# Optimization experiments

Hardware: AMD Instinct MI355X
Metric: run time of the kernel (lower is better)

Reference implementation:

```python
import jax, jax.numpy as jnp
from jax import lax
import numpy as np

H = 180; W = 180            # BEV map: grid_size 1440 / out_size_factor 8
CIN = 384; C = 128; K = 10  # in_channels, hidden_channel, num_classes
P = 200; NH = 8; B = 2      # num_proposals, num_heads, batch
OUT_DIMS = (2, 1, 3, 2, 2, 10)  # center, height, dim, rot, vel, heatmap


def pos2embed(pos, nf=C):
    # faithful to MFFusionHead.pos2embed (note: temperature is unused in source)
    pos = pos * (2.0 * np.pi)
    dim_t = jnp.arange(nf, dtype=pos.dtype)
    dim_t = 2.0 * jnp.floor(dim_t / 2.0) / nf + 1.0
    px = pos[..., 0, None] / dim_t
    py = pos[..., 1, None] / dim_t
    def interleave(p):
        return jnp.stack((jnp.sin(p[..., 0::2]), jnp.cos(p[..., 1::2])), axis=-1).reshape(p.shape[:-1] + (nf,))
    return jnp.concatenate((interleave(py), interleave(px)), axis=-1)  # [..., 2*nf]


def conv2d(t, w, b):
    return lax.conv_general_dilated(t, w, (1, 1), 'SAME', dimension_numbers=('NCHW', 'OIHW', 'NCHW')) + b[None, :, None, None]


def conv1d(t, w, b):
    return lax.conv_general_dilated(t, w, (1,), 'SAME', dimension_numbers=('NCH', 'OIH', 'NCH')) + b[None, :, None]


def layernorm(t, g, b):
    m = t.mean(-1, keepdims=True)
    v = ((t - m) ** 2).mean(-1, keepdims=True)
    return g * (t - m) / jnp.sqrt(v + 1e-5) + b


def mha(q, k, v, w_in, b_in, w_o, b_o):
    Bq, Lq, Cq = q.shape
    d = Cq // NH
    qh = (q @ w_in[0] + b_in[0]).reshape(Bq, Lq, NH, d)
    kh = (k @ w_in[1] + b_in[1]).reshape(Bq, -1, NH, d)
    vh = (v @ w_in[2] + b_in[2]).reshape(Bq, -1, NH, d)
    att = jax.nn.softmax(jnp.einsum('bqhd,bkhd->bhqk', qh, kh) / float(np.sqrt(d)), axis=-1)
    o = jnp.einsum('bhqk,bkhd->bqhd', att, vh).reshape(Bq, Lq, Cq)
    return o @ w_o + b_o


def _forward(x, w_shared, b_shared, w_hm1, b_hm1, g_hm1, beta_hm1, w_hm2, b_hm2,
             w_fp1, b_fp1, g_fp1, beta_fp1, w_fp2, b_fp2,
             w_be1, b_be1, w_be2, b_be2,
             w_attn_s, b_attn_s, w_out_s, b_out_s,
             w_attn_c, b_attn_c, w_out_c, b_out_c,
             ln1_g, ln1_b, ln2_g, ln2_b, ln3_g, ln3_b,
             w_ff1, b_ff1, w_ff2, b_ff2,
             w_head1, b_head1, g_head1, beta_head1, w_head2, b_head2):
    Bx = x.shape[0]
    # shared 3x3 conv over fused BEV features
    feat = conv2d(x, w_shared, b_shared)                      # [B, C, H, W]

    def head2d(w1, b1, g, be, w2, b2):
        h = conv2d(feat, w1, b1)
        h = jax.nn.relu(g[None, :, None, None] * h + be[None, :, None, None])  # BN (eval, affine) + ReLU
        return conv2d(h, w2, b2)

    dense_hm = head2d(w_hm1, b_hm1, g_hm1, beta_hm1, w_hm2, b_hm2)  # [B, K, H, W]
    frontmap = head2d(w_fp1, b_fp1, g_fp1, beta_fp1, w_fp2, b_fp2)  # [B, 1, H, W] (aux output)
    del frontmap

    # local-max NMS on detached sigmoid heatmap
    hm = jax.nn.sigmoid(lax.stop_gradient(dense_hm))
    lm = lax.reduce_window(hm, -jnp.inf, lax.max, (1, 1, 3, 3), (1, 1, 1, 1), 'SAME')
    hm = hm * (hm == lm).astype(hm.dtype)

    # top-k proposal selection across (class, position)
    _, idx = lax.top_k(hm.reshape(Bx, -1), P)                 # [B, P]
    top_idx = idx % (H * W)

    feat_flat = feat.reshape(Bx, C, H * W)

    def gather(a, i):
        return jnp.take_along_axis(a, jnp.broadcast_to(i[:, None, :], (Bx, a.shape[1], P)), axis=2)

    query_feat = gather(feat_flat, top_idx)                   # [B, C, P]
    q_hm_score = gather(hm.reshape(Bx, K, H * W), top_idx)    # [B, K, P]

    # coords_bev grid (+0.5 centers), normalized for sinusoidal embedding
    bev = jnp.stack(jnp.meshgrid(jnp.arange(H, dtype=jnp.float32) + 0.5,
                                 jnp.arange(W, dtype=jnp.float32) + 0.5,
                                 indexing='ij'), axis=-1).reshape(-1, 2)
    bev_n = bev / jnp.asarray([H, W], jnp.float32)

    def emb(p):  # bev_embedding MLP on pos2embed
        return jax.nn.relu(pos2embed(p) @ w_be1 + b_be1) @ w_be2 + b_be2

    qpe = emb(bev_n[top_idx])                                 # [B, P, C]
    kpe = emb(bev_n)[None]                                    # [1, HW, C]

    q = query_feat.transpose(0, 2, 1)                         # [B, P, C]
    mem = feat_flat.transpose(0, 2, 1)                        # [B, HW, C]

    # decoder layer: self-attn -> cross-attn to BEV -> FFN (post-norm)
    q = layernorm(q + mha(q + qpe, q + qpe, q, w_attn_s, b_attn_s, w_out_s, b_out_s), ln1_g, ln1_b)
    q = layernorm(q + mha(q + qpe, mem + kpe, mem, w_attn_c, b_attn_c, w_out_c, b_out_c), ln2_g, ln2_b)
    q = layernorm(q + jax.nn.relu(q @ w_ff1 + b_ff1) @ w_ff2 + b_ff2, ln3_g, ln3_b)

    # SeparateHead prediction (Conv1d k=3 + BN + ReLU + Conv1d)
    qc = q.transpose(0, 2, 1)                                 # [B, C, P]
    outs = []
    for i, od in enumerate(OUT_DIMS):
        h = jax.nn.relu(g_head1[i][None, :, None] * conv1d(qc, w_head1[i], b_head1[i]) + beta_head1[i][None, :, None])
        outs.append(conv1d(h, w_head2[i, :od], b_head2[i, :od]))
    outs[5] = outs[5] + q_hm_score                            # fuse gathered heatmap score into class logits
    return jnp.concatenate(outs, axis=1)                      # [B, 20, P]


def setup_inputs() -> dict:
    key = jax.random.key(0)
    ks = iter(jax.random.split(key, 60))
    def rn(shape, s=0.02):
        return jax.random.normal(next(ks), shape, jnp.float32) * s
    return dict(
        x=jax.random.normal(next(ks), (B, CIN, H, W), jnp.float32),
        w_shared=rn((C, CIN, 3, 3)), b_shared=rn((C,)),
        w_hm1=rn((C, C, 3, 3)), b_hm1=rn((C,)), g_hm1=1.0 + rn((C,)), beta_hm1=rn((C,)),
        w_hm2=rn((K, C, 3, 3)), b_hm2=rn((K,)),
        w_fp1=rn((C, C, 3, 3)), b_fp1=rn((C,)), g_fp1=1.0 + rn((C,)), beta_fp1=rn((C,)),
        w_fp2=rn((1, C, 3, 3)), b_fp2=rn((1,)),
        w_be1=rn((2 * C, C)), b_be1=rn((C,)), w_be2=rn((C, C)), b_be2=rn((C,)),
        w_attn_s=rn((3, C, C)), b_attn_s=rn((3, C)), w_out_s=rn((C, C)), b_out_s=rn((C,)),
        w_attn_c=rn((3, C, C)), b_attn_c=rn((3, C)), w_out_c=rn((C, C)), b_out_c=rn((C,)),
        ln1_g=1.0 + rn((C,)), ln1_b=rn((C,)), ln2_g=1.0 + rn((C,)), ln2_b=rn((C,)),
        ln3_g=1.0 + rn((C,)), ln3_b=rn((C,)),
        w_ff1=rn((C, 2 * C)), b_ff1=rn((2 * C,)), w_ff2=rn((2 * C, C)), b_ff2=rn((C,)),
        w_head1=rn((6, C, C, 3)), b_head1=rn((6, C)), g_head1=1.0 + rn((6, C)), beta_head1=rn((6, C)),
        w_head2=rn((6, K, C, 3)), b_head2=rn((6, K)),
    )


def reference(x, w_shared, b_shared, w_hm1, b_hm1, g_hm1, beta_hm1, w_hm2, b_hm2,
              w_fp1, b_fp1, g_fp1, beta_fp1, w_fp2, b_fp2,
              w_be1, b_be1, w_be2, b_be2,
              w_attn_s, b_attn_s, w_out_s, b_out_s,
              w_attn_c, b_attn_c, w_out_c, b_out_c,
              ln1_g, ln1_b, ln2_g, ln2_b, ln3_g, ln3_b,
              w_ff1, b_ff1, w_ff2, b_ff2,
              w_head1, b_head1, g_head1, beta_head1, w_head2, b_head2):
    return _forward(x, w_shared, b_shared, w_hm1, b_hm1, g_hm1, beta_hm1, w_hm2, b_hm2,
                    w_fp1, b_fp1, g_fp1, beta_fp1, w_fp2, b_fp2,
                    w_be1, b_be1, w_be2, b_be2,
                    w_attn_s, b_attn_s, w_out_s, b_out_s,
                    w_attn_c, b_attn_c, w_out_c, b_out_c,
                    ln1_g, ln1_b, ln2_g, ln2_b, ln3_g, ln3_b,
                    w_ff1, b_ff1, w_ff2, b_ff2,
                    w_head1, b_head1, g_head1, beta_head1, w_head2, b_head2)
```

## Files before the change

kernel.cpp:

```cpp
#include <hip/hip_runtime.h>

#define HH 180
#define WW 180
#define HWN 32400
#define CC 128
#define CINN 384
#define KK 10
#define PP 200
#define NHH 8
#define BB 2
#define NTOT 324000
#define TKBINS (1 << 18)

typedef _Float16 half8 __attribute__((ext_vector_type(8)));
typedef float f32x16 __attribute__((ext_vector_type(16)));

static __device__ __forceinline__ f32x16 MFMA16(half8 a, half8 b, f32x16 c) {
    return __builtin_amdgcn_mfma_f32_32x32x16_f16(a, b, c, 0, 0, 0);
}

__global__ void k_wsplit(const float* __restrict__ w, _Float16* __restrict__ img, int cint) {
    const int e = blockIdx.x * 256 + threadIdx.x;
    const int total = (cint / 32) * 9 * 8192;
    if (e >= total) return;
    const int ii = e & 7, cout = (e >> 3) & 127, q = (e >> 10) & 3, t = (e >> 12) & 1;
    const int bidx = e >> 13, tap = bidx % 9, ch = bidx / 9;
    const int cin = ch * 32 + q * 8 + ii;
    const float v = w[((size_t)cout * cint + cin) * 9 + tap];
    const _Float16 h = (_Float16)v;
    img[e] = (t == 0) ? h : (_Float16)((v - (float)h) * 256.f);
}

__global__ void k_wsplit_hm(const float* __restrict__ w, _Float16* __restrict__ img) {
    const int e = blockIdx.x * 256 + threadIdx.x;
    const int total = 4 * 9 * 2048;
    if (e >= total) return;
    const int ii = e & 7, co = (e >> 3) & 31, q = (e >> 8) & 3, t = (e >> 10) & 1;
    const int bidx = e >> 11, tap = bidx % 9, ch = bidx / 9;
    const int cin = ch * 32 + q * 8 + ii;
    const float v = (co < 10) ? w[((size_t)co * 128 + cin) * 9 + tap] : 0.f;
    const _Float16 h = (_Float16)v;
    img[e] = (t == 0) ? h : (_Float16)((v - (float)h) * 256.f);
}

__global__ __launch_bounds__(256) void k_xsplit(const float* __restrict__ x,
    _Float16* __restrict__ out, int CIN, int NCH)
{
    __shared__ float tile[32][184];
    const int ch = blockIdx.x, y = blockIdx.y, b = blockIdx.z;
    const int tid = threadIdx.x;
    for (int s = tid; s < 32 * 180; s += 256) {
        const int c = s / 180, px = s % 180;
        tile[c][px] = x[(((size_t)b * CIN + ch * 32 + c) * HH + y) * WW + px];
    }
    __syncthreads();
    const size_t pbase = ((((size_t)b * 180 + y) * NCH + ch) * 2) * (180 * 32);
    for (int tt = tid; tt < 1440; tt += 256) {
        const int t = tt / 720, u = tt % 720, px = u >> 2, q = u & 3;
        half8 hv;
#pragma unroll
        for (int j = 0; j < 8; ++j) {
            const float v = tile[q * 8 + j][px];
            const _Float16 h = (_Float16)v;
            hv[j] = (t == 0) ? h : (_Float16)((v - (float)h) * 256.f);
        }
        *(half8*)(out + pbase + (size_t)t * (180 * 32) + px * 32 + q * 8) = hv;
    }
}

template<int NCH, int EPI, int WRITEF, int SPLIT>
__global__ __launch_bounds__(256, 3) void k_conv(
    const _Float16* __restrict__ xs, const _Float16* __restrict__ wimg,
    const float* __restrict__ bias, const float* __restrict__ g,
    const float* __restrict__ beta, float* __restrict__ outf,
    _Float16* __restrict__ outs)
{
    __shared__ __align__(16) char sh[36992];
    const int tid = threadIdx.x;
    const int b = blockIdx.z >> 1, ch2 = blockIdx.z & 1;
    const int oy0 = blockIdx.y * 2, ox0 = blockIdx.x * 64;
    const int wave = tid >> 6, l = tid & 63;
    const int wr = wave >> 1, nh = wave & 1;
    const int l31 = l & 31, kb = l >> 5;

    f32x16 acc1[2] = {};
    f32x16 acc2[2] = {};

    int wofs[2][2];
#pragma unroll
    for (int t = 0; t < 2; ++t)
#pragma unroll
        for (int s = 0; s < 2; ++s)
            wofs[t][s] = (((t * 4) + (s * 2 + kb)) * 128 + ch2 * 64 + nh * 32 + l31) * 16;

    half8 bwC[2][2], bwN[2][2];
#pragma unroll
    for (int t = 0; t < 2; ++t)
#pragma unroll
        for (int s = 0; s < 2; ++s)
            bwC[t][s] = *(const half8*)((const char*)wimg + wofs[t][s]);

#pragma unroll 1
    for (int ch = 0; ch < NCH; ++ch) {
        if (ch) __syncthreads();
#pragma unroll
        for (int k = 0; k < 9; ++k) {
            const int tt = tid + k * 256;
            if (tt < 2112) {
                const int seg = tt / 264, u = tt - seg * 264;
                const int t = seg >> 2, r = seg & 3;
                const int i = u >> 2, q = u & 3;
                const int gy = oy0 - 1 + r, gx = ox0 - 1 + i;
                uint4 v = {0u, 0u, 0u, 0u};
                if ((unsigned)gy < 180u && (unsigned)gx < 180u)
                    v = *(const uint4*)((const char*)xs +
                        (((((size_t)b * 180 + gy) * NCH + ch) * 2 + t) * 180 + gx) * 64 + q * 16);
                *(uint4*)(sh + ((t * 4 + r) * 4 + q) * 1056 + i * 16) = v;
            }
        }
        __syncthreads();
#pragma unroll
        for (int tap = 0; tap < 9; ++tap) {
            const int bidx = ch * 9 + tap;
            const bool pf = (bidx + 1 < NCH * 9);
            if (pf) {
                const char* wn = (const char*)wimg + (size_t)(bidx + 1) * 16384;
#pragma unroll
                for (int t = 0; t < 2; ++t)
#pragma unroll
                    for (int s = 0; s < 2; ++s)
                        bwN[t][s] = *(const half8*)(wn + wofs[t][s]);
            }
            const int ky = tap / 3, kx = tap % 3;
            const int rr = wr + ky;
#pragma unroll
            for (int s = 0; s < 2; ++s) {
                const int q = s * 2 + kb;
                half8 ah[2], al[2];
#pragma unroll
                for (int mf = 0; mf < 2; ++mf) {
                    const int io = (mf * 32 + l31 + kx) * 16;
                    ah[mf] = *(const half8*)(sh + ((rr) * 4 + q) * 1056 + io);
                    al[mf] = *(const half8*)(sh + ((4 + rr) * 4 + q) * 1056 + io);
                }
#pragma unroll
                for (int mf = 0; mf < 2; ++mf) {
                    acc1[mf] = MFMA16(ah[mf], bwC[0][s], acc1[mf]);
                    acc2[mf] = MFMA16(ah[mf], bwC[1][s], acc2[mf]);
                    acc2[mf] = MFMA16(al[mf], bwC[0][s], acc2[mf]);
                }
            }
            if (pf) {
#pragma unroll
                for (int t = 0; t < 2; ++t)
#pragma unroll
                    for (int s = 0; s < 2; ++s)
                        bwC[t][s] = bwN[t][s];
            }
        }
    }

    float* C = (float*)sh;
    const float inv256 = 1.f / 256.f;
    __syncthreads();
#pragma unroll
    for (int mf = 0; mf < 2; ++mf)
#pragma unroll
        for (int reg = 0; reg < 16; ++reg) {
            const int px = mf * 32 + (reg & 3) + 8 * (reg >> 2) + 4 * kb;
            const int co = nh * 32 + l31;
            C[(co * 2 + wr) * 72 + px] = acc1[mf][reg] + acc2[mf][reg] * inv256;
// ... 270 lines not shown
    __shared__ float pe[16][258];
    __shared__ float hid[16][130];
    const int tid = threadIdx.x;
    const int pos0 = blockIdx.x * 16;
    const int half = tid >> 6, m = tid & 63;
    const float dimt = 1.f + (float)m * 0.015625f;
#pragma unroll
    for (int p = 0; p < 16; ++p) {
        const int pos = pos0 + p;
        const int i = pos / WW, j = pos % WW;
        const float coord = (half == 0) ? ((float)j + 0.5f) * (1.f / 180.f)
                                        : ((float)i + 0.5f) * (1.f / 180.f);
        const float arg = (coord * 6.2831855f) / dimt;
        pe[p][half * 128 + 2 * m]     = sinf(arg);
        pe[p][half * 128 + 2 * m + 1] = cosf(arg);
    }
    __syncthreads();
    float acc[16];
#pragma unroll
    for (int p = 0; p < 16; ++p) acc[p] = b1[tid];
    for (int k = 0; k < 256; ++k) {
        const float w = w1[k * 128 + tid];
#pragma unroll
        for (int p = 0; p < 16; ++p) acc[p] += pe[p][k] * w;
    }
#pragma unroll
    for (int p = 0; p < 16; ++p) hid[p][tid] = fmaxf(acc[p], 0.f);
    __syncthreads();
#pragma unroll
    for (int p = 0; p < 16; ++p) acc[p] = b2[tid];
    for (int k = 0; k < 128; ++k) {
        const float w = w2[k * 128 + tid];
#pragma unroll
        for (int p = 0; p < 16; ++p) acc[p] += hid[p][k] * w;
    }
#pragma unroll
    for (int p = 0; p < 16; ++p) kpeT[(size_t)tid * HWN + pos0 + p] = acc[p];
}

__global__ __launch_bounds__(128) void k_gather(const float* __restrict__ feat,
    const float* __restrict__ kpeT, const float* __restrict__ hm_msk,
    const int* __restrict__ top_idx, float* __restrict__ q0,
    float* __restrict__ qpe, float* __restrict__ qhm)
{
    const int p = blockIdx.x, b = blockIdx.y, c = threadIdx.x;
    const int idx = top_idx[b * 200 + p];
    q0[((size_t)b * 200 + p) * 128 + c]  = feat[((size_t)b * 128 + c) * HWN + idx];
    qpe[((size_t)b * 200 + p) * 128 + c] = kpeT[(size_t)c * HWN + idx];
    if (c < 10)
        qhm[((size_t)b * 10 + c) * 200 + p] = hm_msk[((size_t)b * 10 + c) * HWN + idx];
}

__global__ __launch_bounds__(128) void k_proj_self(const float* __restrict__ q0,
    const float* __restrict__ qpe, const float* __restrict__ w,
    const float* __restrict__ bias, float* __restrict__ qh,
    float* __restrict__ kh, float* __restrict__ vh)
{
    __shared__ float in0[128], in1[128];
    const int p = blockIdx.x, b = blockIdx.y, c = threadIdx.x;
    const size_t base = ((size_t)b * 200 + p) * 128;
    const float a = q0[base + c], pe = qpe[base + c];
    in0[c] = a + pe; in1[c] = a;
    __syncthreads();
    float aq = bias[c], ak = bias[128 + c], av = bias[256 + c];
    for (int k = 0; k < 128; ++k) {
        const float i0 = in0[k];
        aq += i0 * w[k * 128 + c];
        ak += i0 * w[16384 + k * 128 + c];
        av += in1[k] * w[32768 + k * 128 + c];
    }
    qh[base + c] = aq; kh[base + c] = ak; vh[base + c] = av;
}

__global__ __launch_bounds__(256) void k_attn_self(const float* __restrict__ qh,
    const float* __restrict__ kh, const float* __restrict__ vh, float* __restrict__ o)
{
    __shared__ float ks[200][16], vs[200][16];
    const int h = blockIdx.x, b = blockIdx.y, tid = threadIdx.x;
    for (int s = tid; s < 3200; s += 256) {
        const int n = s >> 4, d = s & 15;
        ks[n][d] = kh[((size_t)b * 200 + n) * 128 + h * 16 + d];
        vs[n][d] = vh[((size_t)b * 200 + n) * 128 + h * 16 + d];
    }
    __syncthreads();
    if (tid < 200) {
        float q[16];
#pragma unroll
        for (int d = 0; d < 16; ++d)
            q[d] = qh[((size_t)b * 200 + tid) * 128 + h * 16 + d] * 0.25f;
        float mmax = -1e30f, lsum = 0.f, acc[16];
#pragma unroll
        for (int d = 0; d < 16; ++d) acc[d] = 0.f;
        for (int j = 0; j < 200; ++j) {
            float s = 0.f;
#pragma unroll
            for (int d = 0; d < 16; ++d) s += q[d] * ks[j][d];
            const float mn = fmaxf(mmax, s);
            const float corr = __expf(mmax - mn);
            const float pv = __expf(s - mn);
            lsum = lsum * corr + pv;
#pragma unroll
            for (int d = 0; d < 16; ++d) acc[d] = acc[d] * corr + pv * vs[j][d];
            mmax = mn;
        }
#pragma unroll
        for (int d = 0; d < 16; ++d)
            o[((size_t)b * 200 + tid) * 128 + h * 16 + d] = acc[d] / lsum;
    }
}

template<int FUSEQ>
__global__ __launch_bounds__(128) void k_proj_ln(const float* __restrict__ src,
    const float* __restrict__ W, const float* __restrict__ bW,
    const float* __restrict__ resid, const float* __restrict__ g,
    const float* __restrict__ lb, float* __restrict__ out,
    const float* __restrict__ qpe, const float* __restrict__ wq,
    const float* __restrict__ bq, float* __restrict__ qout)
{
    __shared__ float sIn[128];
    __shared__ float rbuf[4];
    __shared__ float lnrow[128];
    const int p = blockIdx.x, b = blockIdx.y, c = threadIdx.x;
    const size_t base = ((size_t)b * 200 + p) * 128;
    sIn[c] = src[base + c];
    __syncthreads();
    float v = bW[c] + resid[base + c];
    for (int k = 0; k < 128; ++k) v += sIn[k] * W[k * 128 + c];
    float s = v;
#pragma unroll
    for (int off = 32; off >= 1; off >>= 1) s += __shfl_xor(s, off);
    if ((c & 63) == 0) rbuf[c >> 6] = s;
    __syncthreads();
    const float mean = (rbuf[0] + rbuf[1]) * (1.f / 128.f);
    const float dv = v - mean;
    float s2 = dv * dv;
#pragma unroll
    for (int off = 32; off >= 1; off >>= 1) s2 += __shfl_xor(s2, off);
    if ((c & 63) == 0) rbuf[2 + (c >> 6)] = s2;
    __syncthreads();
    const float var = (rbuf[2] + rbuf[3]) * (1.f / 128.f);
    const float ln = g[c] * dv / sqrtf(var + 1e-5f) + lb[c];
    out[base + c] = ln;
    if (FUSEQ) {
        lnrow[c] = ln + qpe[base + c];
        __syncthreads();
        float a = bq[c];
        for (int k = 0; k < 128; ++k) a += lnrow[k] * wq[k * 128 + c];
        qout[base + c] = a;
    }
}

__global__ __launch_bounds__(256) void k_kv_cross(const float* __restrict__ feat,
    const float* __restrict__ kpeT, const float* __restrict__ w,
    const float* __restrict__ bias, float* __restrict__ kh, float* __restrict__ vh)
{
    __shared__ float as[32][68];
    __shared__ float wk[32][128], wv[32][128];
    const int tid = threadIdx.x, n0 = blockIdx.x * 64, b = blockIdx.y;
    const int cg = tid & 31, ng = tid >> 5;
    float ak[4][8], av[4][8];
#pragma unroll
    for (int i = 0; i < 4; ++i)
#pragma unroll
        for (int j = 0; j < 8; ++j) { ak[i][j] = 0.f; av[i][j] = 0.f; }
    for (int kc = 0; kc < 128; kc += 32) {
        for (int s = tid; s < 2048; s += 256) {
            const int k = s >> 6, n = s & 63;
            float fv = 0.f;
            if (n0 + n < HWN)
                fv = feat[((size_t)b * 128 + kc + k) * HWN + n0 + n]
                   + kpeT[(size_t)(kc + k) * HWN + n0 + n];
            as[k][n] = fv;
        }
        for (int s = tid; s < 4096; s += 256) {
            const int k = s >> 7, c = s & 127;
            wk[k][c] = w[(128 + kc + k) * 128 + c];
            wv[k][c] = w[(256 + kc + k) * 128 + c];
        }
        __syncthreads();
#pragma unroll
        for (int k = 0; k < 32; ++k) {
            const float4 x0 = *(const float4*)&as[k][ng * 8];
            const float4 x1 = *(const float4*)&as[k][ng * 8 + 4];
            const float4 wk4 = *(const float4*)&wk[k][cg * 4];
            const float4 wv4 = *(const float4*)&wv[k][cg * 4];
            float xv[8] = {x0.x, x0.y, x0.z, x0.w, x1.x, x1.y, x1.z, x1.w};
#pragma unroll
            for (int j = 0; j < 8; ++j) {
                ak[0][j] += wk4.x * xv[j]; ak[1][j] += wk4.y * xv[j];
                ak[2][j] += wk4.z * xv[j]; ak[3][j] += wk4.w * xv[j];
                av[0][j] += wv4.x * xv[j]; av[1][j] += wv4.y * xv[j];
                av[2][j] += wv4.z * xv[j]; av[3][j] += wv4.w * xv[j];
            }
        }
        __syncthreads();
    }
    const float bk0 = bias[128 + cg * 4], bk1 = bias[128 + cg * 4 + 1];
    const float bk2 = bias[128 + cg * 4 + 2], bk3 = bias[128 + cg * 4 + 3];
    const float bv0 = bias[256 + cg * 4], bv1 = bias[256 + cg * 4 + 1];
    const float bv2 = bias[256 + cg * 4 + 2], bv3 = bias[256 + cg * 4 + 3];
#pragma unroll
    for (int j = 0; j < 8; ++j) {
        const int n = n0 + ng * 8 + j;
        if (n < HWN) {
            float4 ko = make_float4(ak[0][j] + bk0, ak[1][j] + bk1, ak[2][j] + bk2, ak[3][j] + bk3);
            float4 vo = make_float4(av[0][j] + bv0, av[1][j] + bv1, av[2][j] + bv2, av[3][j] + bv3);
            *(float4*)(kh + ((size_t)b * HWN + n) * 128 + cg * 4) = ko;
            *(float4*)(vh + ((size_t)b * HWN + n) * 128 + cg * 4) = vo;
        }
    }
}

#define KSPLIT 16
__global__ __launch_bounds__(256) void k_flash(const float* __restrict__ qh,
    const float* __restrict__ kh, const float* __restrict__ vh,
    float* __restrict__ o_part, float* __restrict__ m_part, float* __restrict__ l_part)
{
    __shared__ float ksm[64][16];
    __shared__ float vsm[64][16];
    const int bh = blockIdx.x, rt = blockIdx.y, ksid = blockIdx.z;
    const int b = bh >> 3, h = bh & 7;
    const int tid = threadIdx.x;
    const int wave = tid >> 6, lane = tid & 63;
    const int r2 = lane >> 2, qd = lane & 3;
    const int row0 = rt * 128 + wave * 32 + r2 * 2;
    float q0r[16], q1r[16];
    {
        const bool a0 = row0 < 200, a1 = row0 + 1 < 200;
#pragma unroll
        for (int d = 0; d < 16; ++d) {
            q0r[d] = a0 ? qh[((size_t)b * 200 + row0) * 128 + h * 16 + d] * 0.25f : 0.f;
            q1r[d] = a1 ? qh[((size_t)b * 200 + row0 + 1) * 128 + h * 16 + d] * 0.25f : 0.f;
        }
    }
    const int nBase = ksid * (HWN / KSPLIT), nEnd = nBase + (HWN / KSPLIT);
    float m0 = -1e30f, m1 = -1e30f, l0 = 0.f, l1 = 0.f;
    float acc0[16], acc1[16];
#pragma unroll
    for (int d = 0; d < 16; ++d) { acc0[d] = 0.f; acc1[d] = 0.f; }
    for (int c0 = nBase; c0 < nEnd; c0 += 64) {
        const int cnt = (nEnd - c0 < 64) ? (nEnd - c0) : 64;
        __syncthreads();
        {
            const int n = tid >> 2, d0 = (tid & 3) << 2;
            float4 kv = make_float4(0, 0, 0, 0), vv = make_float4(0, 0, 0, 0);
            if (n < cnt) {
                kv = *(const float4*)(kh + ((size_t)b * HWN + c0 + n) * 128 + h * 16 + d0);
                vv = *(const float4*)(vh + ((size_t)b * HWN + c0 + n) * 128 + h * 16 + d0);
            }
            *(float4*)(&ksm[n][d0]) = kv;
            *(float4*)(&vsm[n][d0]) = vv;
        }
        __syncthreads();
        float s0[16], s1[16];
        float cm0 = -1e30f, cm1 = -1e30f;
#pragma unroll
        for (int jj = 0; jj < 16; ++jj) {
            const int j = (jj << 2) | qd;
            float t0 = 0.f, t1 = 0.f;
#pragma unroll
            for (int d = 0; d < 16; ++d) {
                const float kvv = ksm[j][d];
                t0 += q0r[d] * kvv; t1 += q1r[d] * kvv;
            }
            const bool valid = j < cnt;
            t0 = valid ? t0 : -1e30f;
            t1 = valid ? t1 : -1e30f;
            s0[jj] = t0; s1[jj] = t1;
            cm0 = fmaxf(cm0, t0); cm1 = fmaxf(cm1, t1);
        }
        cm0 = fmaxf(cm0, __shfl_xor(cm0, 1)); cm0 = fmaxf(cm0, __shfl_xor(cm0, 2));
        cm1 = fmaxf(cm1, __shfl_xor(cm1, 1)); cm1 = fmaxf(cm1, __shfl_xor(cm1, 2));
        const float mn0 = fmaxf(m0, cm0), mn1 = fmaxf(m1, cm1);
        const float cr0 = __expf(m0 - mn0), cr1 = __expf(m1 - mn1);
        l0 *= cr0; l1 *= cr1;
#pragma unroll
        for (int d = 0; d < 16; ++d) { acc0[d] *= cr0; acc1[d] *= cr1; }
#pragma unroll
        for (int jj = 0; jj < 16; ++jj) {
            const int j = (jj << 2) | qd;
            const float p0 = __expf(s0[jj] - mn0);
            const float p1 = __expf(s1[jj] - mn1);
            l0 += p0; l1 += p1;
#pragma unroll
            for (int d = 0; d < 16; ++d) {
                const float vvv = vsm[j][d];
                acc0[d] += p0 * vvv; acc1[d] += p1 * vvv;
            }
        }
        m0 = mn0; m1 = mn1;
    }
    l0 += __shfl_xor(l0, 1); l0 += __shfl_xor(l0, 2);
    l1 += __shfl_xor(l1, 1); l1 += __shfl_xor(l1, 2);
#pragma unroll
    for (int d = 0; d < 16; ++d) {
        acc0[d] += __shfl_xor(acc0[d], 1); acc0[d] += __shfl_xor(acc0[d], 2);
        acc1[d] += __shfl_xor(acc1[d], 1); acc1[d] += __shfl_xor(acc1[d], 2);
    }
    if (qd == 0) {
        const size_t pbase = ((size_t)bh * KSPLIT + ksid) * 200;
        if (row0 < 200) {
#pragma unroll
            for (int d = 0; d < 16; ++d) o_part[(pbase + row0) * 16 + d] = acc0[d];
            m_part[pbase + row0] = m0; l_part[pbase + row0] = l0;
        }
        if (row0 + 1 < 200) {
#pragma unroll
            for (int d = 0; d < 16; ++d) o_part[(pbase + row0 + 1) * 16 + d] = acc1[d];
            m_part[pbase + row0 + 1] = m1; l_part[pbase + row0 + 1] = l1;
        }
    }
}

__global__ __launch_bounds__(64) void k_merge(const float* __restrict__ o_part,
    const float* __restrict__ m_part, const float* __restrict__ l_part,
    float* __restrict__ o_c)
{
    const int row = blockIdx.x, bh = blockIdx.y;
    const int b = bh >> 3, h = bh & 7;
    const int lane = threadIdx.x;
    float M = -1e30f;
#pragma unroll
    for (int k = 0; k < KSPLIT; ++k)
        M = fmaxf(M, m_part[((size_t)bh * KSPLIT + k) * 200 + row]);
    float L = 0.f;
#pragma unroll
    for (int k = 0; k < KSPLIT; ++k)
        L += l_part[((size_t)bh * KSPLIT + k) * 200 + row]
           * __expf(m_part[((size_t)bh * KSPLIT + k) * 200 + row] - M);
    if (lane < 16) {
        float o = 0.f;
#pragma unroll
        for (int k = 0; k < KSPLIT; ++k)
            o += o_part[(((size_t)bh * KSPLIT + k) * 200 + row) * 16 + lane]
               * __expf(m_part[((size_t)bh * KSPLIT + k) * 200 + row] - M);
        o_c[((size_t)b * 200 + row) * 128 + h * 16 + lane] = o / L;
    }
}

__global__ __launch_bounds__(256) void k_ffn_ln(const float* __restrict__ x,
    const float* __restrict__ w1, const float* __restrict__ b1,
    const float* __restrict__ w2, const float* __restrict__ b2,
    const float* __restrict__ g, const float* __restrict__ lb, float* __restrict__ out)
{
    __shared__ float xr[128];
    __shared__ float hs[256];
    __shared__ float rbuf[8];
    const int p = blockIdx.x, b = blockIdx.y, t = threadIdx.x;
    const size_t base = ((size_t)b * 200 + p) * 128;
    if (t < 128) xr[t] = x[base + t];
    __syncthreads();
    float hv = b1[t];
    for (int k = 0; k < 128; ++k) hv += xr[k] * w1[k * 256 + t];
    hs[t] = fmaxf(hv, 0.f);
    __syncthreads();
    float v = 0.f;
    if (t < 128) {
        v = b2[t] + xr[t];
        for (int k = 0; k < 256; ++k) v += hs[k] * w2[k * 128 + t];
    }
    float s = (t < 128) ? v : 0.f;
#pragma unroll
    for (int off = 32; off >= 1; off >>= 1) s += __shfl_xor(s, off);
    if ((t & 63) == 0) rbuf[t >> 6] = s;
    __syncthreads();
    const float mean = (rbuf[0] + rbuf[1] + rbuf[2] + rbuf[3]) * (1.f / 128.f);
    const float dv = v - mean;
    float s2 = (t < 128) ? dv * dv : 0.f;
#pragma unroll
    for (int off = 32; off >= 1; off >>= 1) s2 += __shfl_xor(s2, off);
    if ((t & 63) == 0) rbuf[4 + (t >> 6)] = s2;
    __syncthreads();
    const float var = (rbuf[4] + rbuf[5] + rbuf[6] + rbuf[7]) * (1.f / 128.f);
    if (t < 128) out[base + t] = g[t] * dv / sqrtf(var + 1e-5f) + lb[t];
}

__global__ __launch_bounds__(256) void k_head_h(const float* __restrict__ q3,
    const float* __restrict__ w1, const float* __restrict__ b1,
    const float* __restrict__ g, const float* __restrict__ beta,
    float* __restrict__ h_all)
{
    __shared__ float qw[128][32];
    const int pt = blockIdx.x, ih = blockIdx.y, b = blockIdx.z;
    const int tid = threadIdx.x;
    for (int s = tid; s < 4096; s += 256) {
        const int c = s & 127, wg = s >> 7;
        const int pg = pt * 24 - 1 + wg;
        qw[c][wg] = ((unsigned)pg < 200u) ? q3[((size_t)b * 200 + pg) * 128 + c] : 0.f;
    }
    __syncthreads();
    const int c = tid & 127, half = tid >> 7;
    float acc[12];
#pragma unroll
    for (int pp = 0; pp < 12; ++pp) acc[pp] = 0.f;
    const float* wbase = w1 + ((size_t)ih * 128 + c) * 384;
    for (int cin = 0; cin < 128; ++cin) {
        const float4* qp = (const float4*)&qw[cin][half * 12];
        const float4 a0 = qp[0], a1 = qp[1], a2 = qp[2], a3 = qp[3];
        float xr[16] = {a0.x, a0.y, a0.z, a0.w, a1.x, a1.y, a1.z, a1.w,
                        a2.x, a2.y, a2.z, a2.w, a3.x, a3.y, a3.z, a3.w};
        const float w0 = wbase[cin * 3], w1v = wbase[cin * 3 + 1], w2v = wbase[cin * 3 + 2];
#pragma unroll
        for (int pp = 0; pp < 12; ++pp)
            acc[pp] += xr[pp] * w0 + xr[pp + 1] * w1v + xr[pp + 2] * w2v;
    }
    const float bs = b1[ih * 128 + c], gg = g[ih * 128 + c], bt = beta[ih * 128 + c];
#pragma unroll
    for (int pp = 0; pp < 12; ++pp) {
        const int p = pt * 24 + half * 12 + pp;
        if (p < 200)
            h_all[(((size_t)b * 6 + ih) * 128 + c) * 200 + p] =
                fmaxf(gg * (acc[pp] + bs) + bt, 0.f);
    }
}

__global__ void k_head_out(const float* __restrict__ h_all, const float* __restrict__ w2,
    const float* __restrict__ b2, const float* __restrict__ qhm, float* __restrict__ out)
{
    const int gid = blockIdx.x * 256 + threadIdx.x;
    if (gid >= 8000) return;
    const int p = gid % 200, rem = gid / 200, row = rem % 20, b = rem / 20;
    int i, oo;
    if (row < 2)       { i = 0; oo = row; }
    else if (row < 3)  { i = 1; oo = row - 2; }
    else if (row < 6)  { i = 2; oo = row - 3; }
    else if (row < 8)  { i = 3; oo = row - 6; }
    else if (row < 10) { i = 4; oo = row - 8; }
    else               { i = 5; oo = row - 10; }
    const float* hb = h_all + (((size_t)b * 6 + i) * 128) * 200;
    const float* wb = w2 + ((size_t)i * 10 + oo) * 384;
    float acc = b2[i * 10 + oo];
    for (int c = 0; c < 128; ++c) {
        const float* hr = hb + (size_t)c * 200 + p;
        const float x0 = (p > 0) ? hr[-1] : 0.f;
        const float x1 = hr[0];
        const float x2 = (p < 199) ? hr[1] : 0.f;
        acc += x0 * wb[c * 3] + x1 * wb[c * 3 + 1] + x2 * wb[c * 3 + 2];
    }
    if (i == 5) acc += qhm[((size_t)b * 10 + oo) * 200 + p];
    out[((size_t)b * 20 + row) * 200 + p] = acc;
}

extern "C" void kernel_launch(void* const* d_in, const int* in_sizes, int n_in,
                              void* d_out, int out_size, void* d_ws, size_t ws_size,
                              hipStream_t stream) {
    (void)in_sizes; (void)n_in; (void)out_size; (void)ws_size;
    const float* x        = (const float*)d_in[0];
    const float* w_shared = (const float*)d_in[1];
    const float* b_shared = (const float*)d_in[2];
    const float* w_hm1    = (const float*)d_in[3];
    const float* b_hm1    = (const float*)d_in[4];
    const float* g_hm1    = (const float*)d_in[5];
    const float* beta_hm1 = (const float*)d_in[6];
    const float* w_hm2    = (const float*)d_in[7];
    const float* b_hm2    = (const float*)d_in[8];
    const float* w_be1    = (const float*)d_in[15];
    const float* b_be1    = (const float*)d_in[16];
    const float* w_be2    = (const float*)d_in[17];
    const float* b_be2    = (const float*)d_in[18];
    const float* w_attn_s = (const float*)d_in[19];
    const float* b_attn_s = (const float*)d_in[20];
    const float* w_out_s  = (const float*)d_in[21];
    const float* b_out_s  = (const float*)d_in[22];
    const float* w_attn_c = (const float*)d_in[23];
    const float* b_attn_c = (const float*)d_in[24];
    const float* w_out_c  = (const float*)d_in[25];
    const float* b_out_c  = (const float*)d_in[26];
    const float* ln1_g    = (const float*)d_in[27];
    const float* ln1_b    = (const float*)d_in[28];
    const float* ln2_g    = (const float*)d_in[29];
    const float* ln2_b    = (const float*)d_in[30];
    const float* ln3_g    = (const float*)d_in[31];
    const float* ln3_b    = (const float*)d_in[32];
    const float* w_ff1    = (const float*)d_in[33];
    const float* b_ff1    = (const float*)d_in[34];
    const float* w_ff2    = (const float*)d_in[35];
    const float* b_ff2    = (const float*)d_in[36];
    const float* w_head1  = (const float*)d_in[37];
    const float* b_head1  = (const float*)d_in[38];
    const float* g_head1  = (const float*)d_in[39];
    const float* bt_head1 = (const float*)d_in[40];
    const float* w_head2  = (const float*)d_in[41];
    const float* b_head2  = (const float*)d_in[42];

    char* ws = (char*)d_ws;
    size_t off = 0;
    auto alloc = [&](size_t bytes) { size_t o = off; off += (bytes + 255) & ~(size_t)255; return o; };
    _Float16* wimg_s  = (_Float16*)(ws + alloc((size_t)12*9*16384));
    _Float16* wimg_h1 = (_Float16*)(ws + alloc((size_t)4*9*16384));
    _Float16* wimg_hm = (_Float16*)(ws + alloc((size_t)4*9*2048*2));
    char*     xs1reg  = (ws + alloc((size_t)2*180*12*2*180*32*2));
    _Float16* xs1     = (_Float16*)xs1reg;
    _Float16* xs2     = (_Float16*)(ws + alloc((size_t)2*180*4*2*180*32*2));
    float* feat   = (float*)(ws + alloc((size_t)2*128*HWN*4));
    float* bufA   = (float*)(ws + alloc((size_t)2*128*HWN*4));
    float* kpeT   = (float*)(ws + alloc((size_t)128*HWN*4));
    int*   topidx = (int*)  (ws + alloc((size_t)2*200*4));
    unsigned* hist  = (unsigned*)(ws + alloc((size_t)2*TKBINS*4));
    unsigned* pivot = (unsigned*)(ws + alloc((size_t)2*4));
    unsigned long long* cand = (unsigned long long*)(ws + alloc((size_t)2*4096*8));
    unsigned* ccnt  = (unsigned*)(ws + alloc((size_t)2*4));
    float* q0     = (float*)(ws + alloc((size_t)2*200*128*4));
    float* qpe    = (float*)(ws + alloc((size_t)2*200*128*4));
    float* q_hm   = (float*)(ws + alloc((size_t)2*10*200*4));
    float* qh_s   = (float*)(ws + alloc((size_t)2*200*128*4));
    float* kh_s   = (float*)(ws + alloc((size_t)2*200*128*4));
    float* vh_s   = (float*)(ws + alloc((size_t)2*200*128*4));
    float* o_s    = (float*)(ws + alloc((size_t)2*200*128*4));
    float* q1n    = (float*)(ws + alloc((size_t)2*200*128*4));
    float* qh_c   = (float*)(ws + alloc((size_t)2*200*128*4));
    float* o_c    = (float*)(ws + alloc((size_t)2*200*128*4));
    float* q2n    = (float*)(ws + alloc((size_t)2*200*128*4));
    float* q3     = (float*)(ws + alloc((size_t)2*200*128*4));
    float* h_all  = (float*)(ws + alloc((size_t)2*6*128*200*4));

    size_t xo = 0;
    auto xalloc = [&](size_t bytes) { size_t o = xo; xo += (bytes + 255) & ~(size_t)255; return o; };
    float* bufB   = (float*)(xs1reg + xalloc((size_t)2*128*HWN*4));
    float* hm_raw = (float*)(xs1reg + xalloc((size_t)2*10*HWN*4));
    float* hm_msk = (float*)(xs1reg + xalloc((size_t)2*10*HWN*4));
    float* o_part = (float*)(xs1reg + xalloc((size_t)16*KSPLIT*200*16*4));
    float* m_part = (float*)(xs1reg + xalloc((size_t)16*KSPLIT*200*4));
    float* l_part = (float*)(xs1reg + xalloc((size_t)16*KSPLIT*200*4));
    _Float16* h1s = (_Float16*)(xs1reg + xalloc((size_t)2*180*4*2*180*32*2));

    k_tkzero<<<(2*TKBINS)/1024, 1024, 0, stream>>>(hist, ccnt);
    k_wsplit<<<(12*9*8192 + 255)/256, 256, 0, stream>>>(w_shared, wimg_s, CINN);
    k_wsplit<<<(4*9*8192 + 255)/256, 256, 0, stream>>>(w_hm1, wimg_h1, 128);
    k_wsplit_hm<<<(4*9*2048 + 255)/256, 256, 0, stream>>>(w_hm2, wimg_hm);
    k_xsplit<<<dim3(12, 180, 2), 256, 0, stream>>>(x, xs1, CINN, 12);
    k_kpe<<<HWN/16, 128, 0, stream>>>(w_be1, b_be1, w_be2, b_be2, kpeT);
    k_conv<12, 0, 1, 1><<<dim3(3, 90, 4), 256, 0, stream>>>(xs1, wimg_s, b_shared, nullptr, nullptr, feat, xs2);
    k_conv<4, 1, 0, 1><<<dim3(3, 90, 4), 256, 0, stream>>>(xs2, wimg_h1, b_hm1, g_hm1, beta_hm1, nullptr, h1s);
    k_convhm2m<4><<<dim3(3, 90, 2), 256, 0, stream>>>(h1s, wimg_hm, b_hm2, hm_raw);
    k_nms<<<(2*10*HWN + 255)/256, 256, 0, stream>>>(hm_raw, hm_msk, hist);
    k_tkscan<<<2, 1024, 0, stream>>>(hist, pivot);
    k_tkcollect<<<dim3(317, 2), 1024, 0, stream>>>(hm_msk, pivot, cand, ccnt);
    k_tksort<<<2, 1024, 0, stream>>>(cand, ccnt, topidx);
    k_gather<<<dim3(200, 2), 128, 0, stream>>>(feat, kpeT, hm_msk, topidx, q0, qpe, q_hm);
    k_proj_self<<<dim3(200, 2), 128, 0, stream>>>(q0, qpe, w_attn_s, b_attn_s, qh_s, kh_s, vh_s);
    k_attn_self<<<dim3(8, 2), 256, 0, stream>>>(qh_s, kh_s, vh_s, o_s);
    k_proj_ln<1><<<dim3(200, 2), 128, 0, stream>>>(o_s, w_out_s, b_out_s, q0, ln1_g, ln1_b, q1n,
                                                   qpe, w_attn_c, b_attn_c, qh_c);
    k_kv_cross<<<dim3(507, 2), 256, 0, stream>>>(feat, kpeT, w_attn_c, b_attn_c, bufA, bufB);
    k_flash<<<dim3(16, 2, KSPLIT), 256, 0, stream>>>(qh_c, bufA, bufB, o_part, m_part, l_part);
    k_merge<<<dim3(200, 16), 64, 0, stream>>>(o_part, m_part, l_part, o_c);
    k_proj_ln<0><<<dim3(200, 2), 128, 0, stream>>>(o_c, w_out_c, b_out_c, q1n, ln2_g, ln2_b, q2n,
                                                   nullptr, nullptr, nullptr, nullptr);
    k_ffn_ln<<<dim3(200, 2), 256, 0, stream>>>(q2n, w_ff1, b_ff1, w_ff2, b_ff2, ln3_g, ln3_b, q3);
    k_head_h<<<dim3(9, 6, 2), 256, 0, stream>>>(q3, w_head1, b_head1, g_head1, bt_head1, h_all);
    k_head_out<<<32, 256, 0, stream>>>(h_all, w_head2, b_head2, q_hm, (float*)d_out);
}
```

Before: 989.8 us.

## Move cross-attention flash kernel to fp16 split-precision MFMA with head-major K/V layouts

The K/V projection kernel now writes K as per-head fp16 hi/lo pairs and V transposed per head, also as fp16 hi/lo split, replacing the fp32 row-major buffers. The flash kernel is rewritten so one 64-thread wave handles 32 queries and uses 32x32x16 MFMA for both QK^T and PV. Split-precision terms (hi plus lo scaled by 256) keep accuracy close to fp32. Grid size changes to 7x16xKSPLIT. The scalar FMA attention loop and the LDS staging are replaced. The risks are extra MFMA calls for the precision split, P being rounded to fp16, and uncoalesced V loads near the tail.

```diff
diff --git a/kernel.cpp b/kernel.cpp
--- a/kernel.cpp
+++ b/kernel.cpp
@@ -11,12 +11,21 @@
 #define BB 2
 #define NTOT 324000
 #define TKBINS (1 << 18)
+#define KSPLIT 16
 
 typedef _Float16 half8 __attribute__((ext_vector_type(8)));
+typedef _Float16 half4 __attribute__((ext_vector_type(4)));
 typedef float f32x16 __attribute__((ext_vector_type(16)));
+typedef unsigned int u32;
 
 static __device__ __forceinline__ f32x16 MFMA16(half8 a, half8 b, f32x16 c) {
     return __builtin_amdgcn_mfma_f32_32x32x16_f16(a, b, c, 0, 0, 0);
+}
+static __device__ __forceinline__ half8 mkh8(u32 a, u32 b, u32 c, u32 d) {
+    union { u32 u[4]; half8 h; } x; x.u[0] = a; x.u[1] = b; x.u[2] = c; x.u[3] = d; return x.h;
+}
+static __device__ __forceinline__ u32 pkh(float a, float b) {
+    union { _Float16 h[2]; u32 u; } x; x.h[0] = (_Float16)a; x.h[1] = (_Float16)b; return x.u;
 }
 
 __global__ void k_wsplit(const float* __restrict__ w, _Float16* __restrict__ img, int cint) {
@@ -593,7 +602,8 @@
 
 __global__ __launch_bounds__(256) void k_kv_cross(const float* __restrict__ feat,
     const float* __restrict__ kpeT, const float* __restrict__ w,
-    const float* __restrict__ bias, float* __restrict__ kh, float* __restrict__ vh)
+    const float* __restrict__ bias, _Float16* __restrict__ khs,
+    _Float16* __restrict__ vTs)
 {
     __shared__ float as[32][68];
     __shared__ float wk[32][128], wv[32][128];
@@ -636,119 +646,164 @@
         }
         __syncthreads();
     }
-    const float bk0 = bias[128 + cg * 4], bk1 = bias[128 + cg * 4 + 1];
-    const float bk2 = bias[128 + cg * 4 + 2], bk3 = bias[128 + cg * 4 + 3];
-    const float bv0 = bias[256 + cg * 4], bv1 = bias[256 + cg * 4 + 1];
-    const float bv2 = bias[256 + cg * 4 + 2], bv3 = bias[256 + cg * 4 + 3];
+    float bk[4], bv[4];
+#pragma unroll
+    for (int i = 0; i < 4; ++i) {
+        bk[i] = bias[128 + cg * 4 + i];
+        bv[i] = bias[256 + cg * 4 + i];
+    }
+    const int h = cg >> 2;
+    const int d0 = (cg * 4) & 15;
+    const int bh = b * 8 + h;
 #pragma unroll
     for (int j = 0; j < 8; ++j) {
         const int n = n0 + ng * 8 + j;
         if (n < HWN) {
-            float4 ko = make_float4(ak[0][j] + bk0, ak[1][j] + bk1, ak[2][j] + bk2, ak[3][j] + bk3);
-            float4 vo = make_float4(av[0][j] + bv0, av[1][j] + bv1, av[2][j] + bv2, av[3][j] + bv3);
-            *(float4*)(kh + ((size_t)b * HWN + n) * 128 + cg * 4) = ko;
-            *(float4*)(vh + ((size_t)b * HWN + n) * 128 + cg * 4) = vo;
-        }
-    }
-}
-
-#define KSPLIT 16
-__global__ __launch_bounds__(256) void k_flash(const float* __restrict__ qh,
-    const float* __restrict__ kh, const float* __restrict__ vh,
+            half4 kh4, kl4;
+#pragma unroll
+            for (int i = 0; i < 4; ++i) {
+                const float v = ak[i][j] + bk[i];
+                const _Float16 hh = (_Float16)v;
+                kh4[i] = hh;
+                kl4[i] = (_Float16)((v - (float)hh) * 256.f);
+            }
+            _Float16* kp = khs + ((size_t)bh * HWN + n) * 32 + d0;
+            *(half4*)kp = kh4;
+            *(half4*)(kp + 16) = kl4;
+        }
+    }
+    const int nb = n0 + ng * 8;
+#pragma unroll
+    for (int i = 0; i < 4; ++i) {
+        half8 vh8, vl8;
+#pragma unroll
+        for (int j = 0; j < 8; ++j) {
+            const float v = av[i][j] + bv[i];
+            const _Float16 hh = (_Float16)v;
+            vh8[j] = hh;
+            vl8[j] = (_Float16)((v - (float)hh) * 256.f);
+        }
+        _Float16* p0 = vTs + ((size_t)(bh * 2 + 0) * 16 + d0 + i) * HWN + nb;
+        _Float16* p1 = vTs + ((size_t)(bh * 2 + 1) * 16 + d0 + i) * HWN + nb;
+        if (nb + 8 <= HWN) {
+            *(half8*)p0 = vh8;
+            *(half8*)p1 = vl8;
+        } else {
+#pragma unroll
+            for (int j = 0; j < 8; ++j)
+                if (nb + j < HWN) { p0[j] = vh8[j]; p1[j] = vl8[j]; }
+        }
+    }
+}
+
+__global__ __launch_bounds__(64) void k_flash(const float* __restrict__ qh,
+    const _Float16* __restrict__ khs, const _Float16* __restrict__ vTs,
     float* __restrict__ o_part, float* __restrict__ m_part, float* __restrict__ l_part)
 {
-    __shared__ float ksm[64][16];
-    __shared__ float vsm[64][16];
-    const int bh = blockIdx.x, rt = blockIdx.y, ksid = blockIdx.z;
+    const int qt = blockIdx.x, bh = blockIdx.y, ksid = blockIdx.z;
     const int b = bh >> 3, h = bh & 7;
-    const int tid = threadIdx.x;
-    const int wave = tid >> 6, lane = tid & 63;
-    const int r2 = lane >> 2, qd = lane & 3;
-    const int row0 = rt * 128 + wave * 32 + r2 * 2;
-    float q0r[16], q1r[16];
+    const int l = threadIdx.x;
+    const int l31 = l & 31, kb = l >> 5;
+    const int kb4 = kb * 4;
+    const int q = qt * 32 + l31;
+    const float inv256 = 1.f / 256.f;
+
+    half8 qbh, qbl;
     {
-        const bool a0 = row0 < 200, a1 = row0 + 1 < 200;
-#pragma unroll
-        for (int d = 0; d < 16; ++d) {
-            q0r[d] = a0 ? qh[((size_t)b * 200 + row0) * 128 + h * 16 + d] * 0.25f : 0.f;
-            q1r[d] = a1 ? qh[((size_t)b * 200 + row0 + 1) * 128 + h * 16 + d] * 0.25f : 0.f;
-        }
-    }
+        float qv[8];
+        if (q < 200) {
+            const float* qp = qh + ((size_t)b * 200 + q) * 128 + h * 16 + kb * 8;
+#pragma unroll
+            for (int j = 0; j < 8; ++j) qv[j] = qp[j] * 0.25f;
+        } else {
+#pragma unroll
+            for (int j = 0; j < 8; ++j) qv[j] = 0.f;
+        }
+#pragma unroll
+        for (int j = 0; j < 8; ++j) {
+            const _Float16 hh = (_Float16)qv[j];
+            qbh[j] = hh;
+            qbl[j] = (_Float16)((qv[j] - (float)hh) * 256.f);
+        }
+    }
+
     const int nBase = ksid * (HWN / KSPLIT), nEnd = nBase + (HWN / KSPLIT);
-    float m0 = -1e30f, m1 = -1e30f, l0 = 0.f, l1 = 0.f;
-    float acc0[16], acc1[16];
-#pragma unroll
-    for (int d = 0; d < 16; ++d) { acc0[d] = 0.f; acc1[d] = 0.f; }
-    for (int c0 = nBase; c0 < nEnd; c0 += 64) {
-        const int cnt = (nEnd - c0 < 64) ? (nEnd - c0) : 64;
-        __syncthreads();
-        {
-            const int n = tid >> 2, d0 = (tid & 3) << 2;
-            float4 kv = make_float4(0, 0, 0, 0), vv = make_float4(0, 0, 0, 0);
-            if (n < cnt) {
-                kv = *(const float4*)(kh + ((size_t)b * HWN + c0 + n) * 128 + h * 16 + d0);
-                vv = *(const float4*)(vh + ((size_t)b * HWN + c0 + n) * 128 + h * 16 + d0);
-            }
-            *(float4*)(&ksm[n][d0]) = kv;
-            *(float4*)(&vsm[n][d0]) = vv;
-        }
-        __syncthreads();
-        float s0[16], s1[16];
-        float cm0 = -1e30f, cm1 = -1e30f;
-#pragma unroll
-        for (int jj = 0; jj < 16; ++jj) {
-            const int j = (jj << 2) | qd;
-            float t0 = 0.f, t1 = 0.f;
-#pragma unroll
-            for (int d = 0; d < 16; ++d) {
-                const float kvv = ksm[j][d];
-                t0 += q0r[d] * kvv; t1 += q1r[d] * kvv;
-            }
-            const bool valid = j < cnt;
-            t0 = valid ? t0 : -1e30f;
-            t1 = valid ? t1 : -1e30f;
-            s0[jj] = t0; s1[jj] = t1;
-            cm0 = fmaxf(cm0, t0); cm1 = fmaxf(cm1, t1);
-        }
-        cm0 = fmaxf(cm0, __shfl_xor(cm0, 1)); cm0 = fmaxf(cm0, __shfl_xor(cm0, 2));
-        cm1 = fmaxf(cm1, __shfl_xor(cm1, 1)); cm1 = fmaxf(cm1, __shfl_xor(cm1, 2));
-        const float mn0 = fmaxf(m0, cm0), mn1 = fmaxf(m1, cm1);
-        const float cr0 = __expf(m0 - mn0), cr1 = __expf(m1 - mn1);
-        l0 *= cr0; l1 *= cr1;
-#pragma unroll
-        for (int d = 0; d < 16; ++d) { acc0[d] *= cr0; acc1[d] *= cr1; }
-#pragma unroll
-        for (int jj = 0; jj < 16; ++jj) {
-            const int j = (jj << 2) | qd;
-            const float p0 = __expf(s0[jj] - mn0);
-            const float p1 = __expf(s1[jj] - mn1);
-            l0 += p0; l1 += p1;
-#pragma unroll
-            for (int d = 0; d < 16; ++d) {
-                const float vvv = vsm[j][d];
-                acc0[d] += p0 * vvv; acc1[d] += p1 * vvv;
-            }
-        }
-        m0 = mn0; m1 = mn1;
-    }
-    l0 += __shfl_xor(l0, 1); l0 += __shfl_xor(l0, 2);
-    l1 += __shfl_xor(l1, 1); l1 += __shfl_xor(l1, 2);
-#pragma unroll
-    for (int d = 0; d < 16; ++d) {
-        acc0[d] += __shfl_xor(acc0[d], 1); acc0[d] += __shfl_xor(acc0[d], 2);
-        acc1[d] += __shfl_xor(acc1[d], 1); acc1[d] += __shfl_xor(acc1[d], 2);
-    }
-    if (qd == 0) {
-        const size_t pbase = ((size_t)bh * KSPLIT + ksid) * 200;
-        if (row0 < 200) {
-#pragma unroll
-            for (int d = 0; d < 16; ++d) o_part[(pbase + row0) * 16 + d] = acc0[d];
-            m_part[pbase + row0] = m0; l_part[pbase + row0] = l0;
-        }
-        if (row0 + 1 < 200) {
-#pragma unroll
-            for (int d = 0; d < 16; ++d) o_part[(pbase + row0 + 1) * 16 + d] = acc1[d];
-            m_part[pbase + row0 + 1] = m1; l_part[pbase + row0 + 1] = l1;
+    float m = -1e30f, lsum = 0.f;
+    f32x16 acc3 = {}, acc4 = {};
+    const size_t kbase = (size_t)bh * HWN;
+    const size_t vb0 = ((size_t)(bh * 2 + 0) * 16 + l31) * (size_t)HWN;
+    const size_t vb1 = ((size_t)(bh * 2 + 1) * 16 + l31) * (size_t)HWN;
+
+    for (int c0 = nBase; c0 < nEnd; c0 += 32) {
+        int kcol = c0 + l31; if (kcol >= HWN) kcol = HWN - 1;
+        const _Float16* kp = khs + (kbase + kcol) * 32 + kb * 8;
+        const half8 kah = *(const half8*)kp;
+        const half8 kal = *(const half8*)(kp + 16);
+        f32x16 a1 = {}, a2 = {};
+        a1 = MFMA16(kah, qbh, a1);
+        a2 = MFMA16(kah, qbl, a2);
+        a2 = MFMA16(kal, qbh, a2);
+        float s[16];
+        float cm = -1e30f;
+#pragma unroll
+        for (int r = 0; r < 16; ++r) {
+            const int kk = (r & 3) + 8 * (r >> 2) + kb4;
+            float v = a1[r] + a2[r] * inv256;
+            v = (c0 + kk < nEnd) ? v : -1e30f;
+            s[r] = v;
+            cm = fmaxf(cm, v);
+        }
+        cm = fmaxf(cm, __shfl_xor(cm, 32));
+        const float mn = fmaxf(m, cm);
+        const float corr = __expf(m - mn);
+        lsum *= corr;
+#pragma unroll
+        for (int r = 0; r < 16; ++r) { acc3[r] *= corr; acc4[r] *= corr; }
+        float p[16];
+#pragma unroll
+        for (int r = 0; r < 16; ++r) { p[r] = __expf(s[r] - mn); lsum += p[r]; }
+        m = mn;
+        const u32 o01 = pkh(p[0], p[1]),  o23 = pkh(p[2], p[3]);
+        const u32 o45 = pkh(p[4], p[5]),  o67 = pkh(p[6], p[7]);
+        const u32 o89 = pkh(p[8], p[9]),  oAB = pkh(p[10], p[11]);
+        const u32 oCD = pkh(p[12], p[13]), oEF = pkh(p[14], p[15]);
+        const u32 x01 = __shfl_xor(o01, 32), x23 = __shfl_xor(o23, 32);
+        const u32 x45 = __shfl_xor(o45, 32), x67 = __shfl_xor(o67, 32);
+        const u32 x89 = __shfl_xor(o89, 32), xAB = __shfl_xor(oAB, 32);
+        const u32 xCD = __shfl_xor(oCD, 32), xEF = __shfl_xor(oEF, 32);
+        const half8 pb0 = (kb == 0) ? mkh8(o01, o23, x01, x23) : mkh8(x45, x67, o45, o67);
+        const half8 pb1 = (kb == 0) ? mkh8(o89, oAB, x89, xAB) : mkh8(xCD, xEF, oCD, oEF);
+        half8 vh0 = {}, vl0 = {}, vh1 = {}, vl1 = {};
+        if (l31 < 16) {
+            const int cA = c0 + kb * 8;
+            const int cB = c0 + 16 + kb * 8;
+            if (cB + 8 <= HWN) {
+                vh0 = *(const half8*)(vTs + vb0 + cA);
+                vh1 = *(const half8*)(vTs + vb0 + cB);
+                vl0 = *(const half8*)(vTs + vb1 + cA);
+                vl1 = *(const half8*)(vTs + vb1 + cB);
+            } else {
+#pragma unroll
+                for (int j = 0; j < 8; ++j) {
+                    if (cA + j < HWN) { vh0[j] = vTs[vb0 + cA + j]; vl0[j] = vTs[vb1 + cA + j]; }
+                    if (cB + j < HWN) { vh1[j] = vTs[vb0 + cB + j]; vl1[j] = vTs[vb1 + cB + j]; }
+                }
+            }
+        }
+        acc3 = MFMA16(vh0, pb0, acc3);
+        acc3 = MFMA16(vh1, pb1, acc3);
+        acc4 = MFMA16(vl0, pb0, acc4);
+        acc4 = MFMA16(vl1, pb1, acc4);
+    }
+
+    const float lt = lsum + __shfl_xor(lsum, 32);
+    if (q < 200) {
+        const size_t pbase = ((size_t)bh * KSPLIT + ksid) * 200 + q;
+        if (kb == 0) { m_part[pbase] = m; l_part[pbase] = lt; }
+#pragma unroll
+        for (int r = 0; r < 8; ++r) {
+            const int d = (r & 3) + 8 * (r >> 2) + kb4;
+            o_part[pbase * 16 + d] = acc3[r] + acc4[r] * inv256;
         }
     }
 }
@@ -934,7 +989,7 @@
     _Float16* xs1     = (_Float16*)xs1reg;
     _Float16* xs2     = (_Float16*)(ws + alloc((size_t)2*180*4*2*180*32*2));
     float* feat   = (float*)(ws + alloc((size_t)2*128*HWN*4));
-    float* bufA   = (float*)(ws + alloc((size_t)2*128*HWN*4));
+    _Float16* khs = (_Float16*)(ws + alloc((size_t)16*HWN*32*2));
     float* kpeT   = (float*)(ws + alloc((size_t)128*HWN*4));
     int*   topidx = (int*)  (ws + alloc((size_t)2*200*4));
     unsigned* hist  = (unsigned*)(ws + alloc((size_t)2*TKBINS*4));
@@ -957,7 +1012,7 @@
 
     size_t xo = 0;
     auto xalloc = [&](size_t bytes) { size_t o = xo; xo += (bytes + 255) & ~(size_t)255; return o; };
-    float* bufB   = (float*)(xs1reg + xalloc((size_t)2*128*HWN*4));
+    _Float16* vTs = (_Float16*)(xs1reg + xalloc((size_t)16*2*16*HWN*2));
     float* hm_raw = (float*)(xs1reg + xalloc((size_t)2*10*HWN*4));
     float* hm_msk = (float*)(xs1reg + xalloc((size_t)2*10*HWN*4));
     float* o_part = (float*)(xs1reg + xalloc((size_t)16*KSPLIT*200*16*4));
@@ -983,8 +1038,8 @@
     k_attn_self<<<dim3(8, 2), 256, 0, stream>>>(qh_s, kh_s, vh_s, o_s);
     k_proj_ln<1><<<dim3(200, 2), 128, 0, stream>>>(o_s, w_out_s, b_out_s, q0, ln1_g, ln1_b, q1n,
                                                    qpe, w_attn_c, b_attn_c, qh_c);
-    k_kv_cross<<<dim3(507, 2), 256, 0, stream>>>(feat, kpeT, w_attn_c, b_attn_c, bufA, bufB);
-    k_flash<<<dim3(16, 2, KSPLIT), 256, 0, stream>>>(qh_c, bufA, bufB, o_part, m_part, l_part);
+    k_kv_cross<<<dim3(507, 2), 256, 0, stream>>>(feat, kpeT, w_attn_c, b_attn_c, khs, vTs);
+    k_flash<<<dim3(7, 16, KSPLIT), 64, 0, stream>>>(qh_c, khs, vTs, o_part, m_part, l_part);
     k_merge<<<dim3(200, 16), 64, 0, stream>>>(o_part, m_part, l_part, o_c);
     k_proj_ln<0><<<dim3(200, 2), 128, 0, stream>>>(o_c, w_out_c, b_out_c, q1n, ln2_g, ln2_b, q2n,
                                                    nullptr, nullptr, nullptr, nullptr);
```

After: 936.9 us (median of 2 runs). 5.3% less time.
